# Kernel optimization log

Measured on AMD Instinct MI355X. Metric: run time of the kernel, lower is better.

## Reference

```python
import jax, jax.numpy as jnp
import numpy as np

# Per-level grid spatial shapes: ceil([T,H,W]/grid_size/2**i) + 1 with
# video (T,H,W) = (120,1080,1920), grid_size=8, n_levels=2.
GRID_SHAPES = [jnp.array([16.0, 136.0, 241.0], dtype=jnp.float32),
               jnp.array([9.0, 69.0, 121.0], dtype=jnp.float32)]
EMB_DIM = 16
N_PTS = 1_000_000

# 8 binary corner offsets, MSB-first bit order (matches f'{i:03b}').
OFFSETS = jnp.array([[(i >> 2) & 1, (i >> 1) & 1, i & 1] for i in range(8)],
                    dtype=jnp.float32)  # [8,3]


def setup_inputs() -> dict:
    key = jax.random.key(0)
    k0, k1, k2 = jax.random.split(key, 3)
    inputs = jax.random.uniform(k0, (N_PTS, 3), dtype=jnp.float32)
    emb0 = jax.random.normal(k1, (16, 136, 241, EMB_DIM), dtype=jnp.float32)
    emb1 = jax.random.normal(k2, (9, 69, 121, EMB_DIM), dtype=jnp.float32)
    return {"inputs": inputs, "emb0": emb0, "emb1": emb1}


def _encode_level(inputs, emb, gshape):
    # inputs: [N,3] in [0,1]; emb: [T,H,W,D]; gshape: [3] float grid shape
    coords = inputs * (gshape - 1.0)                         # [N,3]
    corner = jnp.floor(coords[:, None, :] + OFFSETS)         # [N,8,3]
    corner = jnp.clip(corner, 0.0, gshape - 1.0)             # [N,8,3]
    idx = corner.astype(jnp.int32)
    values = emb[idx[..., 0], idx[..., 1], idx[..., 2]]      # [N,8,D] gather
    weights = jnp.prod(1.0 - jnp.abs(corner - coords[:, None, :]),
                       axis=-1, keepdims=True)               # [N,8,1]
    return jnp.sum(weights * values, axis=-2)                # [N,D]


def reference(inputs, emb0, emb1):
    out0 = _encode_level(inputs, emb0, GRID_SHAPES[0])
    out1 = _encode_level(inputs, emb1, GRID_SHAPES[1])
    return jnp.concatenate([out0, out1], axis=-1)            # [N, 2*D]
```

## Files before the change

kernel.cpp:

```cpp
#include <hip/hip_runtime.h>


typedef float floatx4 __attribute__((ext_vector_type(4)));

#define KXB 8
#define KYB 17
#define KZB 31
#define NBINS (KXB * KYB * KZB)
#define NSUB 4
#define CAPS 104
#define CAP_TOT (NSUB * CAPS)
#define CNT_DWORDS (NSUB * NBINS + 1)

#define L0X 3
#define L0Y 9
#define L0Z 9
#define L0CELLS (L0X * L0Y * L0Z)
#define L1X 3
#define L1Y 6
#define L1Z 5
#define L1CELLS (L1X * L1Y * L1Z)
#define CSTR 20

__device__ __forceinline__ int point_key(float px, float py, float pz) {
    int ix = (int)(px * 15.0f);  ix = min(max(ix, 0), 15);
    int iy = (int)(py * 135.0f); iy = min(max(iy, 0), 135);
    int iz = (int)(pz * 240.0f); iz = min(max(iz, 0), 240);
    return ((ix >> 1) * KYB + (iy >> 3)) * KZB + (iz >> 3);
}

__device__ __forceinline__ void load4pts(const float* __restrict__ pts, int i4,
                                         float px[4], float py[4], float pz[4]) {
    const floatx4* v = (const floatx4*)(pts + (size_t)i4 * 3);
    const floatx4 a = v[0], b = v[1], c = v[2];
    px[0] = a.x; py[0] = a.y; pz[0] = a.z;
    px[1] = a.w; py[1] = b.x; pz[1] = b.y;
    px[2] = b.z; py[2] = b.w; pz[2] = c.x;
    px[3] = c.y; py[3] = c.z; pz[3] = c.w;
}

__global__ __launch_bounds__(256)
void k_zero(unsigned* __restrict__ cnt) {
    const int i = blockIdx.x * blockDim.x + threadIdx.x;
    if (i < CNT_DWORDS) cnt[i] = 0u;
}

__global__ __launch_bounds__(256)
void k_bin(const float* __restrict__ pts, int n,
           unsigned* __restrict__ cnt, unsigned* __restrict__ ovfc,
           unsigned* __restrict__ slots, unsigned* __restrict__ ovf) {
    const int i4 = (blockIdx.x * blockDim.x + threadIdx.x) * 4;
    if (i4 >= n) return;
    if (i4 + 3 < n) {
        float px[4], py[4], pz[4];
        load4pts(pts, i4, px, py, pz);
        int k[4];
#pragma unroll
        for (int j = 0; j < 4; ++j) k[j] = point_key(px[j], py[j], pz[j]);
        unsigned pos[4];
#pragma unroll
        for (int j = 0; j < 4; ++j)
            pos[j] = atomicAdd(&cnt[j * NBINS + k[j]], 1u);
#pragma unroll
        for (int j = 0; j < 4; ++j) {
            if (pos[j] < CAPS)
                slots[(size_t)k[j] * CAP_TOT + j * CAPS + pos[j]] = (unsigned)(i4 + j);
            else
                ovf[atomicAdd(ovfc, 1u)] = (unsigned)(i4 + j);
        }
    } else {
        for (int j = 0; j < 4 && i4 + j < n; ++j) {
            const size_t b = (size_t)(i4 + j) * 3;
            const int k = point_key(pts[b], pts[b+1], pts[b+2]);
            const unsigned pos = atomicAdd(&cnt[j * NBINS + k], 1u);
            if (pos < CAPS) slots[(size_t)k * CAP_TOT + j * CAPS + pos] = (unsigned)(i4 + j);
            else            ovf[atomicAdd(ovfc, 1u)] = (unsigned)(i4 + j);
        }
    }
}

__device__ __forceinline__ void setup_lds(float cx, float cy, float cz,
                                          float tm1, float hm1, float wm1,
                                          int xb, int yb, int zb,
                                          int ex, int ey, int ez,
                                          int sx, int sy, int d,
                                          int* __restrict__ off,
                                          float* __restrict__ w) {
    float gx[2] = { floorf(cx), floorf(cx + 1.0f) };
    float gy[2] = { floorf(cy), floorf(cy + 1.0f) };
    float gz[2] = { floorf(cz), floorf(cz + 1.0f) };
    float wx[2], wy[2], wz[2];
    int   xo[2], yo[2], zo[2];
#pragma unroll
    for (int b = 0; b < 2; ++b) {
        gx[b] = fminf(fmaxf(gx[b], 0.0f), tm1);
        gy[b] = fminf(fmaxf(gy[b], 0.0f), hm1);
        gz[b] = fminf(fmaxf(gz[b], 0.0f), wm1);
        wx[b] = 1.0f - fabsf(gx[b] - cx);
        wy[b] = 1.0f - fabsf(gy[b] - cy);
        wz[b] = 1.0f - fabsf(gz[b] - cz);
        xo[b] = min((int)gx[b] - xb, ex) * sx;
        yo[b] = min((int)gy[b] - yb, ey) * sy;
        zo[b] = min((int)gz[b] - zb, ez) * CSTR + d;
    }
    float wyz[4];
    int   yzo[4];
#pragma unroll
    for (int j = 0; j < 2; ++j)
#pragma unroll
        for (int k = 0; k < 2; ++k) {
            wyz[2 * j + k] = wy[j] * wz[k];
            yzo[2 * j + k] = yo[j] + zo[k];
        }
#pragma unroll
    for (int c = 0; c < 8; ++c) {
        const int i = (c >> 2) & 1, jk = c & 3;
        w[c]   = wx[i] * wyz[jk];
        off[c] = xo[i] + yzo[jk];
    }
}

__device__ __forceinline__ void setup_glb(float cx, float cy, float cz,
                                          float tm1, float hm1, float wm1,
                                          int sh, int sw, int d,
                                          int* __restrict__ off,
                                          float* __restrict__ w) {
    float gx[2] = { floorf(cx), floorf(cx + 1.0f) };
    float gy[2] = { floorf(cy), floorf(cy + 1.0f) };
    float gz[2] = { floorf(cz), floorf(cz + 1.0f) };
    float wx[2], wy[2], wz[2];
    int   xo[2], yo[2], zo[2];
#pragma unroll
    for (int b = 0; b < 2; ++b) {
        gx[b] = fminf(fmaxf(gx[b], 0.0f), tm1);
        gy[b] = fminf(fmaxf(gy[b], 0.0f), hm1);
        gz[b] = fminf(fmaxf(gz[b], 0.0f), wm1);
        wx[b] = 1.0f - fabsf(gx[b] - cx);
        wy[b] = 1.0f - fabsf(gy[b] - cy);
        wz[b] = 1.0f - fabsf(gz[b] - cz);
        xo[b] = (int)gx[b] * sh;
        yo[b] = (int)gy[b] * sw;
        zo[b] = (int)gz[b] * 16 + d;
    }
    float wyz[4];
    int   yzo[4];
#pragma unroll
    for (int j = 0; j < 2; ++j)
#pragma unroll
        for (int k = 0; k < 2; ++k) {
            wyz[2 * j + k] = wy[j] * wz[k];
            yzo[2 * j + k] = yo[j] + zo[k];
        }
#pragma unroll
    for (int c = 0; c < 8; ++c) {
        const int i = (c >> 2) & 1, jk = c & 3;
        w[c]   = wx[i] * wyz[jk];
        off[c] = xo[i] + yzo[jk];
    }
}

__device__ __forceinline__ void encode_glb_quad(int p, int lane4,
                                                const float* __restrict__ pts,
                                                const float* __restrict__ emb0,
                                                const float* __restrict__ emb1,
                                                float* __restrict__ out) {
    const size_t b = (size_t)p * 3;
    const float px = pts[b], py = pts[b + 1], pz = pts[b + 2];
    int   o0[8], o1[8];
    float w0[8], w1[8];
    setup_glb(px * 15.0f, py * 135.0f, pz * 240.0f, 15.0f, 135.0f, 240.0f,
              136 * 241 * 16, 241 * 16, lane4, o0, w0);
    setup_glb(px * 8.0f, py * 68.0f, pz * 120.0f, 8.0f, 68.0f, 120.0f,
              69 * 121 * 16, 121 * 16, lane4, o1, w1);
    floatx4 a0 = {0,0,0,0}, a1 = {0,0,0,0};
#pragma unroll
    for (int c = 0; c < 8; ++c) a0 += w0[c] * *(const floatx4*)(emb0 + o0[c]);
#pragma unroll
    for (int c = 0; c < 8; ++c) a1 += w1[c] * *(const floatx4*)(emb1 + o1[c]);
    float* row = out + (size_t)p * 32 + lane4;
    __builtin_nontemporal_store(a0, (floatx4*)row);
    __builtin_nontemporal_store(a1, (floatx4*)(row + 16));
}

__global__ __launch_bounds__(256, 6)
void k_main_bins(const unsigned* __restrict__ slots,
                 const unsigned* __restrict__ cnt,
                 const unsigned* __restrict__ ovfc,
                 const unsigned* __restrict__ ovf,
                 const float* __restrict__ pts,
                 const float* __restrict__ emb0,
                 const float* __restrict__ emb1,
                 float* __restrict__ out) {
    const int bin = (blockIdx.x & 7) * 527 + (blockIdx.x >> 3);
    const unsigned n0 = min(cnt[bin],             (unsigned)CAPS);
    const unsigned n1 = min(cnt[NBINS + bin],     (unsigned)CAPS);
    const unsigned n2 = min(cnt[2 * NBINS + bin], (unsigned)CAPS);
    const unsigned n3 = min(cnt[3 * NBINS + bin], (unsigned)CAPS);
    const unsigned c0 = n0, c1 = c0 + n1, c2 = c1 + n2, nt = c2 + n3;

    __shared__ float lds0[L0CELLS * CSTR];
    __shared__ float lds1[L1CELLS * CSTR];

    const int tid = threadIdx.x;
    const int d = (tid & 3) * 4;

    if (nt != 0) {
        const int bz = bin % KZB;
        const int t1 = bin / KZB;
        const int by = t1 % KYB;
        const int bx = t1 / KYB;

        const int x0 = bx * 2, y0 = by * 8, z0 = bz * 8;
        const int x1b = bx, y1b = (544 * by) / 135, z1b = bz * 4;

        for (int idx = tid; idx < L0CELLS * 4; idx += 256) {
            const int cell = idx >> 2, q = (idx & 3) * 4;
            const int lz = cell % L0Z;
            const int t = cell / L0Z;
            const int ly = t % L0Y, lx = t / L0Y;
            const int gx = min(x0 + lx, 15), gy = min(y0 + ly, 135), gz = min(z0 + lz, 240);
            const floatx4 v = *(const floatx4*)(emb0 + ((size_t)(gx * 136 + gy) * 241 + gz) * 16 + q);
            *(floatx4*)(lds0 + cell * CSTR + q) = v;
        }
        for (int idx = tid; idx < L1CELLS * 4; idx += 256) {
            const int cell = idx >> 2, q = (idx & 3) * 4;
            const int lz = cell % L1Z;
            const int t = cell / L1Z;
            const int ly = t % L1Y, lx = t / L1Y;
            const int gx = min(x1b + lx, 8), gy = min(y1b + ly, 68), gz = min(z1b + lz, 120);
            const floatx4 v = *(const floatx4*)(emb1 + ((size_t)(gx * 69 + gy) * 121 + gz) * 16 + q);
            *(floatx4*)(lds1 + cell * CSTR + q) = v;
        }
        __syncthreads();

        const int quad = tid >> 2;
        const size_t sbase = (size_t)bin * CAP_TOT;

        auto slot_of = [&](unsigned t) -> unsigned {
            const unsigned seg = (t >= c0) + (t >= c1) + (t >= c2);
            const unsigned base = (seg == 0) ? 0u : ((seg == 1) ? c0 : ((seg == 2) ? c1 : c2));
            return (unsigned)(sbase + seg * CAPS + (t - base));
        };

        unsigned tA = quad, tB = quad + 64;
        int origA = (int)slots[slot_of(min(tA, nt - 1))];
        int origB = (int)slots[slot_of(min(tB, nt - 1))];
        size_t pbA = (size_t)origA * 3;
        float pxA = pts[pbA], pyA = pts[pbA + 1], pzA = pts[pbA + 2];

        while (tA < nt) {
            const unsigned tC = tB + 64;
            const int origC = (int)slots[slot_of(min(tC, nt - 1))];
            const size_t pbB = (size_t)origB * 3;
            const float pxB = pts[pbB], pyB = pts[pbB + 1], pzB = pts[pbB + 2];

            int   o0[8], o1[8];
            float w0[8], w1[8];
            setup_lds(pxA * 15.0f, pyA * 135.0f, pzA * 240.0f, 15.0f, 135.0f, 240.0f,
                      x0, y0, z0, L0X - 1, L0Y - 1, L0Z - 1,
                      L0Y * L0Z * CSTR, L0Z * CSTR, d, o0, w0);
            setup_lds(pxA * 8.0f, pyA * 68.0f, pzA * 120.0f, 8.0f, 68.0f, 120.0f,
                      x1b, y1b, z1b, L1X - 1, L1Y - 1, L1Z - 1,
                      L1Y * L1Z * CSTR, L1Z * CSTR, d, o1, w1);

            floatx4 a0 = {0.f, 0.f, 0.f, 0.f}, a1 = {0.f, 0.f, 0.f, 0.f};
#pragma unroll
            for (int c = 0; c < 8; ++c) a0 += w0[c] * *(const floatx4*)(lds0 + o0[c]);
#pragma unroll
            for (int c = 0; c < 8; ++c) a1 += w1[c] * *(const floatx4*)(lds1 + o1[c]);

            float* row = out + (size_t)origA * 32 + d;
            __builtin_nontemporal_store(a0, (floatx4*)row);
            __builtin_nontemporal_store(a1, (floatx4*)(row + 16));

            tA = tB; tB = tC;
            origA = origB; origB = origC;
            pxA = pxB; pyA = pyB; pzA = pzB;
        }
    }

    if (blockIdx.x < 64) {
        const unsigned total = *ovfc;
        for (unsigned i = (blockIdx.x * 256 + tid) >> 2; i < total;
             i += (64u * 256u) >> 2) {
            encode_glb_quad((int)ovf[i], d, pts, emb0, emb1, out);
        }
    }
}

__global__ __launch_bounds__(256)
void k_main_plain(const float* __restrict__ pts,
                  const float* __restrict__ emb0,
                  const float* __restrict__ emb1,
                  float* __restrict__ out, int n) {
    const int g = blockIdx.x * blockDim.x + threadIdx.x;
    const int p = g >> 2;
    if (p >= n) return;
    encode_glb_quad(p, (g & 3) * 4, pts, emb0, emb1, out);
}

extern "C" void kernel_launch(void* const* d_in, const int* in_sizes, int n_in,
                              void* d_out, int out_size, void* d_ws, size_t ws_size,
                              hipStream_t stream) {
    const float* pts  = (const float*)d_in[0];
    const float* emb0 = (const float*)d_in[1];
    const float* emb1 = (const float*)d_in[2];
    float* out = (float*)d_out;
    const int n = in_sizes[0] / 3;

    const int block = 256;
    const int n4      = (n + 3) / 4;
    const int grid_p4 = (n4 + block - 1) / block;
    const int grid_4l = (int)(((long long)n * 4 + block - 1) / block);
    const int grid_z  = (CNT_DWORDS + block - 1) / block;

    const size_t off_cnt   = 0;
    const size_t off_ovfc  = (size_t)NSUB * NBINS * 4;
    const size_t off_slots = ((off_ovfc + 4 + 31) & ~(size_t)31);
    const size_t off_ovf   = off_slots + (size_t)NBINS * CAP_TOT * 4;
    const size_t need      = off_ovf + (size_t)n * 4;

    if (ws_size < need) {
        k_main_plain<<<grid_4l, block, 0, stream>>>(pts, emb0, emb1, out, n);
        return;
    }

    char* ws = (char*)d_ws;
    unsigned* cnt   = (unsigned*)(ws + off_cnt);
    unsigned* ovfc  = (unsigned*)(ws + off_ovfc);
    unsigned* slots = (unsigned*)(ws + off_slots);
    unsigned* ovf   = (unsigned*)(ws + off_ovf);

    k_zero<<<grid_z, block, 0, stream>>>(cnt);
    k_bin<<<grid_p4, block, 0, stream>>>(pts, n, cnt, ovfc, slots, ovf);
    k_main_bins<<<NBINS, block, 0, stream>>>(slots, cnt, ovfc, ovf,
                                             pts, emb0, emb1, out);
}
```

Measured before the change: 114.0 us.

## Gather level-1 embeddings from global memory instead of staging them in LDS

Removes the level-1 LDS tile and its staging loop. Level-1 corners are now read straight from global memory (the small level-1 table should stay cache-resident), and those loads are issued before the level-0 LDS reads, with a scheduling barrier so they overlap. setup_lds is specialized to level-0 constants, and the launch-bounds occupancy hint drops from 6 to 4 to leave more registers for the eight in-flight level-1 vectors. The trade is less LDS use and no staging work per block against global-load latency on every point and lower minimum occupancy.

```diff
diff --git a/kernel.cpp b/kernel.cpp
--- a/kernel.cpp
+++ b/kernel.cpp
@@ -16,10 +16,6 @@
 #define L0Y 9
 #define L0Z 9
 #define L0CELLS (L0X * L0Y * L0Z)
-#define L1X 3
-#define L1Y 6
-#define L1Z 5
-#define L1CELLS (L1X * L1Y * L1Z)
 #define CSTR 20
 
 __device__ __forceinline__ int point_key(float px, float py, float pz) {
@@ -80,10 +76,7 @@
 }
 
 __device__ __forceinline__ void setup_lds(float cx, float cy, float cz,
-                                          float tm1, float hm1, float wm1,
-                                          int xb, int yb, int zb,
-                                          int ex, int ey, int ez,
-                                          int sx, int sy, int d,
+                                          int xb, int yb, int zb, int d,
                                           int* __restrict__ off,
                                           float* __restrict__ w) {
     float gx[2] = { floorf(cx), floorf(cx + 1.0f) };
@@ -93,15 +86,15 @@
     int   xo[2], yo[2], zo[2];
 #pragma unroll
     for (int b = 0; b < 2; ++b) {
-        gx[b] = fminf(fmaxf(gx[b], 0.0f), tm1);
-        gy[b] = fminf(fmaxf(gy[b], 0.0f), hm1);
-        gz[b] = fminf(fmaxf(gz[b], 0.0f), wm1);
+        gx[b] = fminf(fmaxf(gx[b], 0.0f), 15.0f);
+        gy[b] = fminf(fmaxf(gy[b], 0.0f), 135.0f);
+        gz[b] = fminf(fmaxf(gz[b], 0.0f), 240.0f);
         wx[b] = 1.0f - fabsf(gx[b] - cx);
         wy[b] = 1.0f - fabsf(gy[b] - cy);
         wz[b] = 1.0f - fabsf(gz[b] - cz);
-        xo[b] = min((int)gx[b] - xb, ex) * sx;
-        yo[b] = min((int)gy[b] - yb, ey) * sy;
-        zo[b] = min((int)gz[b] - zb, ez) * CSTR + d;
+        xo[b] = min((int)gx[b] - xb, L0X - 1) * (L0Y * L0Z * CSTR);
+        yo[b] = min((int)gy[b] - yb, L0Y - 1) * (L0Z * CSTR);
+        zo[b] = min((int)gz[b] - zb, L0Z - 1) * CSTR + d;
     }
     float wyz[4];
     int   yzo[4];
@@ -182,7 +175,7 @@
     __builtin_nontemporal_store(a1, (floatx4*)(row + 16));
 }
 
-__global__ __launch_bounds__(256, 6)
+__global__ __launch_bounds__(256, 4)
 void k_main_bins(const unsigned* __restrict__ slots,
                  const unsigned* __restrict__ cnt,
                  const unsigned* __restrict__ ovfc,
@@ -199,7 +192,6 @@
     const unsigned c0 = n0, c1 = c0 + n1, c2 = c1 + n2, nt = c2 + n3;
 
     __shared__ float lds0[L0CELLS * CSTR];
-    __shared__ float lds1[L1CELLS * CSTR];
 
     const int tid = threadIdx.x;
     const int d = (tid & 3) * 4;
@@ -211,7 +203,6 @@
         const int bx = t1 / KYB;
 
         const int x0 = bx * 2, y0 = by * 8, z0 = bz * 8;
-        const int x1b = bx, y1b = (544 * by) / 135, z1b = bz * 4;
 
         for (int idx = tid; idx < L0CELLS * 4; idx += 256) {
             const int cell = idx >> 2, q = (idx & 3) * 4;
@@ -222,15 +213,6 @@
             const floatx4 v = *(const floatx4*)(emb0 + ((size_t)(gx * 136 + gy) * 241 + gz) * 16 + q);
             *(floatx4*)(lds0 + cell * CSTR + q) = v;
         }
-        for (int idx = tid; idx < L1CELLS * 4; idx += 256) {
-            const int cell = idx >> 2, q = (idx & 3) * 4;
-            const int lz = cell % L1Z;
-            const int t = cell / L1Z;
-            const int ly = t % L1Y, lx = t / L1Y;
-            const int gx = min(x1b + lx, 8), gy = min(y1b + ly, 68), gz = min(z1b + lz, 120);
-            const floatx4 v = *(const floatx4*)(emb1 + ((size_t)(gx * 69 + gy) * 121 + gz) * 16 + q);
-            *(floatx4*)(lds1 + cell * CSTR + q) = v;
-        }
         __syncthreads();
 
         const int quad = tid >> 2;
@@ -256,18 +238,20 @@
 
             int   o0[8], o1[8];
             float w0[8], w1[8];
-            setup_lds(pxA * 15.0f, pyA * 135.0f, pzA * 240.0f, 15.0f, 135.0f, 240.0f,
-                      x0, y0, z0, L0X - 1, L0Y - 1, L0Z - 1,
-                      L0Y * L0Z * CSTR, L0Z * CSTR, d, o0, w0);
-            setup_lds(pxA * 8.0f, pyA * 68.0f, pzA * 120.0f, 8.0f, 68.0f, 120.0f,
-                      x1b, y1b, z1b, L1X - 1, L1Y - 1, L1Z - 1,
-                      L1Y * L1Z * CSTR, L1Z * CSTR, d, o1, w1);
+            setup_lds(pxA * 15.0f, pyA * 135.0f, pzA * 240.0f, x0, y0, z0, d, o0, w0);
+            setup_glb(pxA * 8.0f, pyA * 68.0f, pzA * 120.0f, 8.0f, 68.0f, 120.0f,
+                      69 * 121 * 16, 121 * 16, d, o1, w1);
+
+            floatx4 v1[8];
+#pragma unroll
+            for (int c = 0; c < 8; ++c) v1[c] = *(const floatx4*)(emb1 + o1[c]);
+            __builtin_amdgcn_sched_barrier(0);
 
             floatx4 a0 = {0.f, 0.f, 0.f, 0.f}, a1 = {0.f, 0.f, 0.f, 0.f};
 #pragma unroll
             for (int c = 0; c < 8; ++c) a0 += w0[c] * *(const floatx4*)(lds0 + o0[c]);
 #pragma unroll
-            for (int c = 0; c < 8; ++c) a1 += w1[c] * *(const floatx4*)(lds1 + o1[c]);
+            for (int c = 0; c < 8; ++c) a1 += w1[c] * v1[c];
 
             float* row = out + (size_t)origA * 32 + d;
             __builtin_nontemporal_store(a0, (floatx4*)row);
```

Result: faster. 111.3 us (-2.4%).
